# Optimization experiments

Hardware: AMD Instinct MI355X
Metric: run time of the kernel (lower is better)

The kernel has to match this reference:

```python
import jax, jax.numpy as jnp
from jax import lax
import numpy as np

B, L, D = 32, 128, 6          # programs, statements per program, tree depth
T = 2 ** D - 1                # nodes per statement tree (complete binary tree)
V, E, C, H = 50000, 128, 128, 256  # vocab, embed dim, encode dim, gru hidden


def setup_inputs():
    key = jax.random.key(0)
    ks = jax.random.split(key, 12)
    s = 0.05
    return {
        "tokens": jax.random.randint(ks[0], (B, L, T), 0, V),
        "emb": jax.random.normal(ks[1], (V, E), jnp.float32) * s,
        "Wc": jax.random.normal(ks[2], (C, E), jnp.float32) * s,
        "bc": jax.random.normal(ks[3], (C,), jnp.float32) * s,
        "Wih_f": jax.random.normal(ks[4], (3 * H, C), jnp.float32) * s,
        "Whh_f": jax.random.normal(ks[5], (3 * H, H), jnp.float32) * s,
        "bih_f": jax.random.normal(ks[6], (3 * H,), jnp.float32) * s,
        "bhh_f": jax.random.normal(ks[7], (3 * H,), jnp.float32) * s,
        "Wih_b": jax.random.normal(ks[8], (3 * H, C), jnp.float32) * s,
        "Whh_b": jax.random.normal(ks[9], (3 * H, H), jnp.float32) * s,
        "bih_b": jax.random.normal(ks[10], (3 * H,), jnp.float32) * s,
        "bhh_b": jax.random.normal(ks[11], (3 * H,), jnp.float32) * s,
    }


def _tree_encode(tokens, emb, Wc, bc):
    # h(node) = W_c(embed(tok)) + sum of children subtree encodings (W_l/W_r unused in source)
    h = jnp.einsum("blte,ce->bltc", emb[tokens], Wc) + bc  # [B,L,T,C]
    for d in range(D - 1, 0, -1):  # deepest level first
        start, n = 2 ** d - 1, 2 ** d
        ch = h[:, :, start:start + n, :]
        ch = ch.reshape(ch.shape[0], ch.shape[1], n // 2, 2, ch.shape[-1]).sum(3)
        p0 = 2 ** (d - 1) - 1
        h = h.at[:, :, p0:p0 + n // 2, :].add(ch)
    # max over all subtree encodings, with zeros included (batch_node starts at 0)
    return jnp.maximum(h.max(axis=2), 0.0)  # [B,L,C]


def _gru_dir(x, Wih, Whh, bih, bhh, reverse):
    # torch GRU gate order: r, z, n
    def step(hp, xt):
        gi = xt @ Wih.T + bih
        gh = hp @ Whh.T + bhh
        ir, iz, inn = jnp.split(gi, 3, -1)
        hr, hz, hn = jnp.split(gh, 3, -1)
        r = jax.nn.sigmoid(ir + hr)
        z = jax.nn.sigmoid(iz + hz)
        nn_ = jnp.tanh(inn + r * hn)
        hnew = (1.0 - z) * nn_ + z * hp
        return hnew, hnew
    xs = jnp.swapaxes(x, 0, 1)  # [L,B,C]
    h0 = jnp.zeros((x.shape[0], Whh.shape[1]), x.dtype)
    _, ys = lax.scan(step, h0, xs, reverse=reverse)
    return jnp.swapaxes(ys, 0, 1)  # [B,L,H]


def reference(tokens, emb, Wc, bc, Wih_f, Whh_f, bih_f, bhh_f, Wih_b, Whh_b, bih_b, bhh_b):
    enc = _tree_encode(tokens, emb, Wc, bc)                       # [B,L,C]
    fwd = _gru_dir(enc, Wih_f, Whh_f, bih_f, bhh_f, reverse=False)
    bwd = _gru_dir(enc, Wih_b, Whh_b, bih_b, bhh_b, reverse=True)
    gru_out = jnp.concatenate([fwd, bwd], axis=-1)                # [B,L,2H]
    return gru_out.max(axis=1)                                    # max-pool over time -> [B,2H]
```

## Files before the change

kernel.cpp:

```cpp
#include <hip/hip_runtime.h>
#include <hip/hip_bf16.h>
#include <hip/hip_fp16.h>
#include <math.h>

#define NV 50000
#define NC 128
#define NH 256
#define NB 32
#define NL 128
#define NT 63
#define G3 768

typedef _Float16 half2_t __attribute__((ext_vector_type(2)));

__device__ __forceinline__ float sigmoidf_(float x) { return 1.0f / (1.0f + expf(-x)); }

__device__ __forceinline__ float fdot2_(unsigned int a, unsigned int b, float c) {
#if __has_builtin(__builtin_amdgcn_fdot2)
  return __builtin_amdgcn_fdot2(__builtin_bit_cast(half2_t, a),
                                __builtin_bit_cast(half2_t, b), c, false);
#else
  half2_t ah = __builtin_bit_cast(half2_t, a);
  half2_t bh = __builtin_bit_cast(half2_t, b);
  return fmaf((float)ah[0], (float)bh[0], fmaf((float)ah[1], (float)bh[1], c));
#endif
}

__global__ __launch_bounds__(256) void gemm_bt_k128(
    const float* __restrict__ A, const float* __restrict__ Bm,
    const float* __restrict__ bias, float* __restrict__ Cm,
    int M, int N) {
  __shared__ __align__(16) float As[64 * 129];
  __shared__ __align__(16) float BsT[128 * 132];
  const int m0 = blockIdx.x * 64;
  const int n0 = blockIdx.y * 128;
  const int tid = threadIdx.x;

#pragma unroll
  for (int i = 0; i < 32; ++i) {
    int e = tid + i * 256;
    int r = e >> 7, k = e & 127;
    int m = m0 + r;
    As[r * 129 + k] = (m < M) ? A[(size_t)m * 128 + k] : 0.0f;
  }
#pragma unroll
  for (int i = 0; i < 64; ++i) {
    int e = tid + i * 256;
    int n = e >> 7, k = e & 127;
    BsT[k * 132 + n] = Bm[(size_t)(n0 + n) * 128 + k];
  }
  __syncthreads();

  const int tn = tid & 15;
  const int tm = tid >> 4;
  const int ml = tm * 4, nl = tn * 8;

  float acc[4][8];
#pragma unroll
  for (int i = 0; i < 4; ++i)
#pragma unroll
    for (int j = 0; j < 8; ++j) acc[i][j] = 0.0f;

#pragma unroll 4
  for (int k = 0; k < 128; ++k) {
    float a0 = As[(ml + 0) * 129 + k];
    float a1 = As[(ml + 1) * 129 + k];
    float a2 = As[(ml + 2) * 129 + k];
    float a3 = As[(ml + 3) * 129 + k];
    float4 b0 = *(const float4*)&BsT[k * 132 + nl];
    float4 b1 = *(const float4*)&BsT[k * 132 + nl + 4];
    const float bv[8] = {b0.x, b0.y, b0.z, b0.w, b1.x, b1.y, b1.z, b1.w};
#pragma unroll
    for (int j = 0; j < 8; ++j) {
      acc[0][j] = fmaf(a0, bv[j], acc[0][j]);
      acc[1][j] = fmaf(a1, bv[j], acc[1][j]);
      acc[2][j] = fmaf(a2, bv[j], acc[2][j]);
      acc[3][j] = fmaf(a3, bv[j], acc[3][j]);
    }
  }

  float bv[8];
#pragma unroll
  for (int j = 0; j < 8; ++j) bv[j] = bias ? bias[n0 + nl + j] : 0.0f;

#pragma unroll
  for (int i = 0; i < 4; ++i) {
    int m = m0 + ml + i;
    if (m < M) {
      float* crow = &Cm[(size_t)m * N + n0 + nl];
#pragma unroll
      for (int j = 0; j < 8; ++j) crow[j] = acc[i][j] + bv[j];
    }
  }
}

__global__ __launch_bounds__(256) void gemm_bt_k128_dual(
    const float* __restrict__ A,
    const float* __restrict__ B0, const float* __restrict__ B1,
    const float* __restrict__ bias0, const float* __restrict__ bias1,
    float* __restrict__ C0, float* __restrict__ C1, int M, int N) {
  const float* __restrict__ Bm = blockIdx.z ? B1 : B0;
  const float* __restrict__ bias = blockIdx.z ? bias1 : bias0;
  float* __restrict__ Cm = blockIdx.z ? C1 : C0;

  __shared__ __align__(16) float As[64 * 129];
  __shared__ __align__(16) float BsT[128 * 132];
  const int m0 = blockIdx.x * 64;
  const int n0 = blockIdx.y * 128;
  const int tid = threadIdx.x;

#pragma unroll
  for (int i = 0; i < 32; ++i) {
    int e = tid + i * 256;
    int r = e >> 7, k = e & 127;
    int m = m0 + r;
    As[r * 129 + k] = (m < M) ? A[(size_t)m * 128 + k] : 0.0f;
  }
#pragma unroll
  for (int i = 0; i < 64; ++i) {
    int e = tid + i * 256;
    int n = e >> 7, k = e & 127;
    BsT[k * 132 + n] = Bm[(size_t)(n0 + n) * 128 + k];
  }
  __syncthreads();

  const int tn = tid & 15;
  const int tm = tid >> 4;
  const int ml = tm * 4, nl = tn * 8;

  float acc[4][8];
#pragma unroll
  for (int i = 0; i < 4; ++i)
#pragma unroll
    for (int j = 0; j < 8; ++j) acc[i][j] = 0.0f;

#pragma unroll 4
  for (int k = 0; k < 128; ++k) {
    float a0 = As[(ml + 0) * 129 + k];
    float a1 = As[(ml + 1) * 129 + k];
    float a2 = As[(ml + 2) * 129 + k];
    float a3 = As[(ml + 3) * 129 + k];
    float4 b0 = *(const float4*)&BsT[k * 132 + nl];
    float4 b1 = *(const float4*)&BsT[k * 132 + nl + 4];
    const float bv[8] = {b0.x, b0.y, b0.z, b0.w, b1.x, b1.y, b1.z, b1.w};
#pragma unroll
    for (int j = 0; j < 8; ++j) {
      acc[0][j] = fmaf(a0, bv[j], acc[0][j]);
      acc[1][j] = fmaf(a1, bv[j], acc[1][j]);
      acc[2][j] = fmaf(a2, bv[j], acc[2][j]);
      acc[3][j] = fmaf(a3, bv[j], acc[3][j]);
    }
  }

  float bv[8];
#pragma unroll
  for (int j = 0; j < 8; ++j) bv[j] = bias[n0 + nl + j];

#pragma unroll
  for (int i = 0; i < 4; ++i) {
    int m = m0 + ml + i;
    if (m < M) {
      float* crow = &Cm[(size_t)m * N + n0 + nl];
#pragma unroll
      for (int j = 0; j < 8; ++j) crow[j] = acc[i][j] + bv[j];
    }
  }
}

__global__ __launch_bounds__(128) void tree_encode(
    const int* __restrict__ tokens, const float* __restrict__ P,
    const float* __restrict__ bc, float* __restrict__ enc) {
  __shared__ int toks[NT];
  const int blk = blockIdx.x;
  const int c = threadIdx.x;
  if (c < NT) toks[c] = tokens[(size_t)blk * NT + c];
  __syncthreads();

  float s[NT];
#pragma unroll
  for (int i = 0; i < NT; ++i) s[i] = P[(size_t)toks[i] * NC + c];
#pragma unroll
  for (int i = 30; i >= 0; --i) s[i] += s[2 * i + 1] + s[2 * i + 2];

  const float bcv = bc[c];
  float m = -1e30f;
#pragma unroll
  for (int i = 0; i < NT; ++i) {
    const float cnt = (i == 0) ? 63.0f
                    : (i < 3)  ? 31.0f
                    : (i < 7)  ? 15.0f
                    : (i < 15) ? 7.0f
                    : (i < 31) ? 3.0f
                               : 1.0f;
    m = fmaxf(m, s[i] + cnt * bcv);
  }
  enc[(size_t)blk * NC + c] = fmaxf(m, 0.0f);
}

__global__ __launch_bounds__(256) void conv_w_pack(
    const float* __restrict__ Wf, const float* __restrict__ Wb,
    uint4* __restrict__ out) {
  int i = blockIdx.x * 256 + threadIdx.x;
  if (i >= 2 * 32 * G3) return;
  int dir = i / (32 * G3);
  int rem = i - dir * 32 * G3;
  int kc = rem / G3;
  int row = rem - kc * G3;
  const float* __restrict__ W = dir ? Wb : Wf;
  const float4 a = *(const float4*)&W[(size_t)row * NH + kc * 8];
  const float4 b = *(const float4*)&W[(size_t)row * NH + kc * 8 + 4];
  __half2 p0 = __floats2half2_rn(a.x, a.y);
  __half2 p1 = __floats2half2_rn(a.z, a.w);
  __half2 p2 = __floats2half2_rn(b.x, b.y);
  __half2 p3 = __floats2half2_rn(b.z, b.w);
  uint4 o;
  o.x = *(unsigned int*)&p0; o.y = *(unsigned int*)&p1;
  o.z = *(unsigned int*)&p2; o.w = *(unsigned int*)&p3;
  out[i] = o;
}

__global__ __launch_bounds__(512, 2) void gru_scan_v4(
    const uint4* __restrict__ Wpk, const float* __restrict__ GI,
    const float* __restrict__ bhh_f, const float* __restrict__ bhh_b,
    float* __restrict__ out) {
  const int dir = blockIdx.x >> 5;
  const int b = blockIdx.x & 31;
  const int tid = threadIdx.x;
  const int c = tid >> 1;
  const int kh = tid & 1;

  __shared__ __align__(16) uint4 hbuf[2][32];

  const uint4* __restrict__ Wd = Wpk + (size_t)dir * 32 * G3;
  uint4 wr[16], wz[16], wn[16];
#pragma unroll
  for (int j = 0; j < 16; ++j) {
    const size_t base = (size_t)(kh * 16 + j) * G3 + c;
    wr[j] = Wd[base];
    wz[j] = Wd[base + NH];
    wn[j] = Wd[base + 2 * NH];
  }
  const float* __restrict__ bhh = dir ? bhh_b : bhh_f;
  const float br = bhh[c], bz = bhh[c + NH], bn = bhh[c + 2 * NH];
  if (tid < 32) ((uint4*)hbuf)[tid] = uint4{0u, 0u, 0u, 0u};

  const float* __restrict__ gi_base =
      GI + ((size_t)dir * NB * NL + (size_t)b * NL) * G3;
  float gir, giz, gin;
  {
    const float* g = gi_base + (size_t)(dir ? NL - 1 : 0) * G3;
    gir = g[c]; giz = g[c + NH]; gin = g[c + 2 * NH];
  }
  float hreg = 0.0f, hmax = -1e30f;
  __syncthreads();

  for (int st = 0; st < NL; ++st) {
    float girN, gizN, ginN;
    {
      const int stn = (st + 1 < NL) ? st + 1 : st;
      const int tn = dir ? (NL - 1 - stn) : stn;
      const float* g = gi_base + (size_t)tn * G3;
      girN = g[c]; gizN = g[c + NH]; ginN = g[c + 2 * NH];
    }
    const uint4* __restrict__ h4 = hbuf[st & 1] + kh * 16;
    float ar = 0.f, az = 0.f, an = 0.f;
#pragma unroll
    for (int j = 0; j < 16; ++j) {
      uint4 hv = h4[j];
      ar = fdot2_(wr[j].x, hv.x, ar); ar = fdot2_(wr[j].y, hv.y, ar);
      ar = fdot2_(wr[j].z, hv.z, ar); ar = fdot2_(wr[j].w, hv.w, ar);
      az = fdot2_(wz[j].x, hv.x, az); az = fdot2_(wz[j].y, hv.y, az);
      az = fdot2_(wz[j].z, hv.z, az); az = fdot2_(wz[j].w, hv.w, az);
      an = fdot2_(wn[j].x, hv.x, an); an = fdot2_(wn[j].y, hv.y, an);
      an = fdot2_(wn[j].z, hv.z, an); an = fdot2_(wn[j].w, hv.w, an);
    }
    ar += __shfl_xor(ar, 1);
    az += __shfl_xor(az, 1);
    an += __shfl_xor(an, 1);
    float r = sigmoidf_(gir + ar + br);
    float z = sigmoidf_(giz + az + bz);
    float n = tanhf(gin + r * (an + bn));
    hreg = (1.0f - z) * n + z * hreg;
    hmax = fmaxf(hmax, hreg);
    if (kh == 0) {
      ((unsigned short*)hbuf[(st + 1) & 1])[c] =
          __half_as_ushort(__float2half_rn(hreg));
    }
    __syncthreads();
    gir = girN; giz = gizN; gin = ginN;
  }
  if (kh == 0) out[(size_t)b * (2 * NH) + (size_t)dir * NH + c] = hmax;
}

extern "C" void kernel_launch(void* const* d_in, const int* in_sizes, int n_in,
                              void* d_out, int out_size, void* d_ws, size_t ws_size,
                              hipStream_t stream) {
  const int*   tokens = (const int*)d_in[0];
  const float* emb    = (const float*)d_in[1];
  const float* Wc     = (const float*)d_in[2];
  const float* bc     = (const float*)d_in[3];
  const float* Wih_f  = (const float*)d_in[4];
  const float* Whh_f  = (const float*)d_in[5];
  const float* bih_f  = (const float*)d_in[6];
  const float* bhh_f  = (const float*)d_in[7];
  const float* Wih_b  = (const float*)d_in[8];
  const float* Whh_b  = (const float*)d_in[9];
  const float* bih_b  = (const float*)d_in[10];
  const float* bhh_b  = (const float*)d_in[11];
  float* out = (float*)d_out;

  float* P   = (float*)d_ws;
  float* enc = P + (size_t)NV * NC;
  float* GI  = enc + (size_t)NB * NL * NC;
  uint4* Wpk = (uint4*)(GI + (size_t)2 * NB * NL * G3);

  conv_w_pack<<<dim3((2 * 32 * G3 + 255) / 256), dim3(256), 0, stream>>>(
      Whh_f, Whh_b, Wpk);
  gemm_bt_k128<<<dim3((NV + 63) / 64, NC / 128), dim3(256), 0, stream>>>(
      emb, Wc, nullptr, P, NV, NC);
  tree_encode<<<dim3(NB * NL), dim3(128), 0, stream>>>(tokens, P, bc, enc);
  gemm_bt_k128_dual<<<dim3(NB * NL / 64, G3 / 128, 2), dim3(256), 0, stream>>>(
      enc, Wih_f, Wih_b, bih_f, bih_b,
      GI, GI + (size_t)NB * NL * G3, NB * NL, G3);
  gru_scan_v4<<<dim3(64), dim3(512), 0, stream>>>(
      Wpk, GI, bhh_f, bhh_b, out);
}
```

Baseline: 324.3 us.

## Restructure GRU scan to 4-way K split with DPP reductions and halve GEMM LDS

The GRU recurrence kernel changes from 2 threads per hidden unit to 4 threads per pair of hidden units, each covering a quarter of K for two output columns. Partial sums are reduced with DPP lane swizzles instead of shuffles, and the LDS hidden buffer is padded to avoid bank conflicts. The weight-pack kernel is rewritten to match the new register layout. The GEMM kernels stage B in two 64-wide K halves, halving B's LDS so more blocks can be resident, at the cost of an extra barrier.

```diff
diff --git a/kernel.cpp b/kernel.cpp
--- a/kernel.cpp
+++ b/kernel.cpp
@@ -26,12 +26,23 @@
 #endif
 }
 
+__device__ __forceinline__ float dpp_xor1_add(float v) {
+  int x = __builtin_amdgcn_update_dpp(0, __builtin_bit_cast(int, v),
+                                      0xB1 , 0xF, 0xF, true);
+  return v + __builtin_bit_cast(float, x);
+}
+__device__ __forceinline__ float dpp_xor2_add(float v) {
+  int x = __builtin_amdgcn_update_dpp(0, __builtin_bit_cast(int, v),
+                                      0x4E , 0xF, 0xF, true);
+  return v + __builtin_bit_cast(float, x);
+}
+
 __global__ __launch_bounds__(256) void gemm_bt_k128(
     const float* __restrict__ A, const float* __restrict__ Bm,
     const float* __restrict__ bias, float* __restrict__ Cm,
     int M, int N) {
   __shared__ __align__(16) float As[64 * 129];
-  __shared__ __align__(16) float BsT[128 * 132];
+  __shared__ __align__(16) float BsT[64 * 132];
   const int m0 = blockIdx.x * 64;
   const int n0 = blockIdx.y * 128;
   const int tid = threadIdx.x;
@@ -43,13 +54,6 @@
     int m = m0 + r;
     As[r * 129 + k] = (m < M) ? A[(size_t)m * 128 + k] : 0.0f;
   }
-#pragma unroll
-  for (int i = 0; i < 64; ++i) {
-    int e = tid + i * 256;
-    int n = e >> 7, k = e & 127;
-    BsT[k * 132 + n] = Bm[(size_t)(n0 + n) * 128 + k];
-  }
-  __syncthreads();
 
   const int tn = tid & 15;
   const int tm = tid >> 4;
@@ -61,21 +65,33 @@
 #pragma unroll
     for (int j = 0; j < 8; ++j) acc[i][j] = 0.0f;
 
+#pragma unroll
+  for (int h = 0; h < 2; ++h) {
+    if (h) __syncthreads();
+#pragma unroll
+    for (int i = 0; i < 32; ++i) {
+      int e = tid + i * 256;
+      int n = e >> 6, kk = e & 63;
+      BsT[kk * 132 + n] = Bm[(size_t)(n0 + n) * 128 + h * 64 + kk];
+    }
+    __syncthreads();
 #pragma unroll 4
-  for (int k = 0; k < 128; ++k) {
-    float a0 = As[(ml + 0) * 129 + k];
-    float a1 = As[(ml + 1) * 129 + k];
-    float a2 = As[(ml + 2) * 129 + k];
-    float a3 = As[(ml + 3) * 129 + k];
-    float4 b0 = *(const float4*)&BsT[k * 132 + nl];
-    float4 b1 = *(const float4*)&BsT[k * 132 + nl + 4];
-    const float bv[8] = {b0.x, b0.y, b0.z, b0.w, b1.x, b1.y, b1.z, b1.w};
-#pragma unroll
-    for (int j = 0; j < 8; ++j) {
-      acc[0][j] = fmaf(a0, bv[j], acc[0][j]);
-      acc[1][j] = fmaf(a1, bv[j], acc[1][j]);
-      acc[2][j] = fmaf(a2, bv[j], acc[2][j]);
-      acc[3][j] = fmaf(a3, bv[j], acc[3][j]);
+    for (int kk = 0; kk < 64; ++kk) {
+      const int k = h * 64 + kk;
+      float a0 = As[(ml + 0) * 129 + k];
+      float a1 = As[(ml + 1) * 129 + k];
+      float a2 = As[(ml + 2) * 129 + k];
+      float a3 = As[(ml + 3) * 129 + k];
+      float4 b0 = *(const float4*)&BsT[kk * 132 + nl];
+      float4 b1 = *(const float4*)&BsT[kk * 132 + nl + 4];
+      const float bv[8] = {b0.x, b0.y, b0.z, b0.w, b1.x, b1.y, b1.z, b1.w};
+#pragma unroll
+      for (int j = 0; j < 8; ++j) {
+        acc[0][j] = fmaf(a0, bv[j], acc[0][j]);
+        acc[1][j] = fmaf(a1, bv[j], acc[1][j]);
+        acc[2][j] = fmaf(a2, bv[j], acc[2][j]);
+        acc[3][j] = fmaf(a3, bv[j], acc[3][j]);
+      }
     }
   }
 
@@ -104,7 +120,7 @@
   float* __restrict__ Cm = blockIdx.z ? C1 : C0;
 
   __shared__ __align__(16) float As[64 * 129];
-  __shared__ __align__(16) float BsT[128 * 132];
+  __shared__ __align__(16) float BsT[64 * 132];
   const int m0 = blockIdx.x * 64;
   const int n0 = blockIdx.y * 128;
   const int tid = threadIdx.x;
@@ -116,13 +132,6 @@
     int m = m0 + r;
     As[r * 129 + k] = (m < M) ? A[(size_t)m * 128 + k] : 0.0f;
   }
-#pragma unroll
-  for (int i = 0; i < 64; ++i) {
-    int e = tid + i * 256;
-    int n = e >> 7, k = e & 127;
-    BsT[k * 132 + n] = Bm[(size_t)(n0 + n) * 128 + k];
-  }
-  __syncthreads();
 
   const int tn = tid & 15;
   const int tm = tid >> 4;
@@ -134,21 +143,33 @@
 #pragma unroll
     for (int j = 0; j < 8; ++j) acc[i][j] = 0.0f;
 
+#pragma unroll
+  for (int h = 0; h < 2; ++h) {
+    if (h) __syncthreads();
+#pragma unroll
+    for (int i = 0; i < 32; ++i) {
+      int e = tid + i * 256;
+      int n = e >> 6, kk = e & 63;
+      BsT[kk * 132 + n] = Bm[(size_t)(n0 + n) * 128 + h * 64 + kk];
+    }
+    __syncthreads();
 #pragma unroll 4
-  for (int k = 0; k < 128; ++k) {
-    float a0 = As[(ml + 0) * 129 + k];
-    float a1 = As[(ml + 1) * 129 + k];
-    float a2 = As[(ml + 2) * 129 + k];
-    float a3 = As[(ml + 3) * 129 + k];
-    float4 b0 = *(const float4*)&BsT[k * 132 + nl];
-    float4 b1 = *(const float4*)&BsT[k * 132 + nl + 4];
-    const float bv[8] = {b0.x, b0.y, b0.z, b0.w, b1.x, b1.y, b1.z, b1.w};
-#pragma unroll
-    for (int j = 0; j < 8; ++j) {
-      acc[0][j] = fmaf(a0, bv[j], acc[0][j]);
-      acc[1][j] = fmaf(a1, bv[j], acc[1][j]);
-      acc[2][j] = fmaf(a2, bv[j], acc[2][j]);
-      acc[3][j] = fmaf(a3, bv[j], acc[3][j]);
+    for (int kk = 0; kk < 64; ++kk) {
+      const int k = h * 64 + kk;
+      float a0 = As[(ml + 0) * 129 + k];
+      float a1 = As[(ml + 1) * 129 + k];
+      float a2 = As[(ml + 2) * 129 + k];
+      float a3 = As[(ml + 3) * 129 + k];
+      float4 b0 = *(const float4*)&BsT[kk * 132 + nl];
+      float4 b1 = *(const float4*)&BsT[kk * 132 + nl + 4];
+      const float bv[8] = {b0.x, b0.y, b0.z, b0.w, b1.x, b1.y, b1.z, b1.w};
+#pragma unroll
+      for (int j = 0; j < 8; ++j) {
+        acc[0][j] = fmaf(a0, bv[j], acc[0][j]);
+        acc[1][j] = fmaf(a1, bv[j], acc[1][j]);
+        acc[2][j] = fmaf(a2, bv[j], acc[2][j]);
+        acc[3][j] = fmaf(a3, bv[j], acc[3][j]);
+      }
     }
   }
 
@@ -201,11 +222,17 @@
     const float* __restrict__ Wf, const float* __restrict__ Wb,
     uint4* __restrict__ out) {
   int i = blockIdx.x * 256 + threadIdx.x;
-  if (i >= 2 * 32 * G3) return;
-  int dir = i / (32 * G3);
-  int rem = i - dir * 32 * G3;
-  int kc = rem / G3;
-  int row = rem - kc * G3;
+  if (i >= 2 * 48 * 512) return;
+  const int dir = i / (48 * 512);
+  int rem = i - dir * (48 * 512);
+  const int jj = rem >> 9;
+  const int gq = rem & 511;
+  const int g = gq >> 2;
+  const int q = gq & 3;
+  const int rowSel = jj >> 3;
+  const int j = jj & 7;
+  const int row = (rowSel % 3) * 256 + (rowSel / 3) * 128 + g;
+  const int kc = q * 8 + j;
   const float* __restrict__ W = dir ? Wb : Wf;
   const float4 a = *(const float4*)&W[(size_t)row * NH + kc * 8];
   const float4 b = *(const float4*)&W[(size_t)row * NH + kc * 8 + 4];
@@ -219,77 +246,91 @@
   out[i] = o;
 }
 
-__global__ __launch_bounds__(512, 2) void gru_scan_v4(
+__global__ __launch_bounds__(512, 2) void gru_scan_v5(
     const uint4* __restrict__ Wpk, const float* __restrict__ GI,
     const float* __restrict__ bhh_f, const float* __restrict__ bhh_b,
     float* __restrict__ out) {
   const int dir = blockIdx.x >> 5;
   const int b = blockIdx.x & 31;
   const int tid = threadIdx.x;
-  const int c = tid >> 1;
-  const int kh = tid & 1;
-
-  __shared__ __align__(16) uint4 hbuf[2][32];
-
-  const uint4* __restrict__ Wd = Wpk + (size_t)dir * 32 * G3;
-  uint4 wr[16], wz[16], wn[16];
-#pragma unroll
-  for (int j = 0; j < 16; ++j) {
-    const size_t base = (size_t)(kh * 16 + j) * G3 + c;
-    wr[j] = Wd[base];
-    wz[j] = Wd[base + NH];
-    wn[j] = Wd[base + 2 * NH];
-  }
+  const int g = tid >> 2;
+  const int q = tid & 3;
+
+  __shared__ __align__(16) unsigned short hbuf[2][288];
+
+  const uint4* __restrict__ Wd = Wpk + (size_t)dir * 48 * 512;
+  uint4 w[48];
+#pragma unroll
+  for (int jj = 0; jj < 48; ++jj) w[jj] = Wd[(size_t)jj * 512 + tid];
+
+  const bool owner = ((q & 1) == 0);
+  const int c = g + (q >> 1) * 128;
   const float* __restrict__ bhh = dir ? bhh_b : bhh_f;
-  const float br = bhh[c], bz = bhh[c + NH], bn = bhh[c + 2 * NH];
-  if (tid < 32) ((uint4*)hbuf)[tid] = uint4{0u, 0u, 0u, 0u};
+  float br = 0.f, bz = 0.f, bn = 0.f;
+  if (owner) {
+    br = bhh[c]; bz = bhh[c + NH]; bn = bhh[c + 2 * NH];
+  }
+  if (tid < 144) ((unsigned int*)&hbuf[0][0])[tid] = 0u;
 
   const float* __restrict__ gi_base =
       GI + ((size_t)dir * NB * NL + (size_t)b * NL) * G3;
-  float gir, giz, gin;
-  {
-    const float* g = gi_base + (size_t)(dir ? NL - 1 : 0) * G3;
-    gir = g[c]; giz = g[c + NH]; gin = g[c + 2 * NH];
+  float gir = 0.f, giz = 0.f, gin = 0.f;
+  if (owner) {
+    const float* gi = gi_base + (size_t)(dir ? NL - 1 : 0) * G3;
+    gir = gi[c]; giz = gi[c + NH]; gin = gi[c + 2 * NH];
   }
   float hreg = 0.0f, hmax = -1e30f;
   __syncthreads();
 
   for (int st = 0; st < NL; ++st) {
-    float girN, gizN, ginN;
-    {
+    float girN = 0.f, gizN = 0.f, ginN = 0.f;
+    if (owner) {
       const int stn = (st + 1 < NL) ? st + 1 : st;
-      const int tn = dir ? (NL - 1 - stn) : stn;
-      const float* g = gi_base + (size_t)tn * G3;
-      girN = g[c]; gizN = g[c + NH]; ginN = g[c + 2 * NH];
-    }
-    const uint4* __restrict__ h4 = hbuf[st & 1] + kh * 16;
-    float ar = 0.f, az = 0.f, an = 0.f;
-#pragma unroll
-    for (int j = 0; j < 16; ++j) {
-      uint4 hv = h4[j];
-      ar = fdot2_(wr[j].x, hv.x, ar); ar = fdot2_(wr[j].y, hv.y, ar);
-      ar = fdot2_(wr[j].z, hv.z, ar); ar = fdot2_(wr[j].w, hv.w, ar);
-      az = fdot2_(wz[j].x, hv.x, az); az = fdot2_(wz[j].y, hv.y, az);
-      az = fdot2_(wz[j].z, hv.z, az); az = fdot2_(wz[j].w, hv.w, az);
-      an = fdot2_(wn[j].x, hv.x, an); an = fdot2_(wn[j].y, hv.y, an);
-      an = fdot2_(wn[j].z, hv.z, an); an = fdot2_(wn[j].w, hv.w, an);
-    }
-    ar += __shfl_xor(ar, 1);
-    az += __shfl_xor(az, 1);
-    an += __shfl_xor(an, 1);
-    float r = sigmoidf_(gir + ar + br);
-    float z = sigmoidf_(giz + az + bz);
-    float n = tanhf(gin + r * (an + bn));
-    hreg = (1.0f - z) * n + z * hreg;
-    hmax = fmaxf(hmax, hreg);
-    if (kh == 0) {
-      ((unsigned short*)hbuf[(st + 1) & 1])[c] =
+      const int t = dir ? (NL - 1 - stn) : stn;
+      const float* gi = gi_base + (size_t)t * G3;
+      girN = gi[c]; gizN = gi[c + NH]; ginN = gi[c + 2 * NH];
+    }
+    const uint4* __restrict__ hp =
+        (const uint4*)((const char*)&hbuf[st & 1][0] + q * 144);
+    float a0 = 0.f, a1 = 0.f, a2 = 0.f, a3 = 0.f, a4 = 0.f, a5 = 0.f;
+#pragma unroll
+    for (int j = 0; j < 8; ++j) {
+      uint4 hv = hp[j];
+      a0 = fdot2_(w[j].x, hv.x, a0);      a0 = fdot2_(w[j].y, hv.y, a0);
+      a0 = fdot2_(w[j].z, hv.z, a0);      a0 = fdot2_(w[j].w, hv.w, a0);
+      a1 = fdot2_(w[8+j].x, hv.x, a1);    a1 = fdot2_(w[8+j].y, hv.y, a1);
+      a1 = fdot2_(w[8+j].z, hv.z, a1);    a1 = fdot2_(w[8+j].w, hv.w, a1);
+      a2 = fdot2_(w[16+j].x, hv.x, a2);   a2 = fdot2_(w[16+j].y, hv.y, a2);
+      a2 = fdot2_(w[16+j].z, hv.z, a2);   a2 = fdot2_(w[16+j].w, hv.w, a2);
+      a3 = fdot2_(w[24+j].x, hv.x, a3);   a3 = fdot2_(w[24+j].y, hv.y, a3);
+      a3 = fdot2_(w[24+j].z, hv.z, a3);   a3 = fdot2_(w[24+j].w, hv.w, a3);
+      a4 = fdot2_(w[32+j].x, hv.x, a4);   a4 = fdot2_(w[32+j].y, hv.y, a4);
+      a4 = fdot2_(w[32+j].z, hv.z, a4);   a4 = fdot2_(w[32+j].w, hv.w, a4);
+      a5 = fdot2_(w[40+j].x, hv.x, a5);   a5 = fdot2_(w[40+j].y, hv.y, a5);
+      a5 = fdot2_(w[40+j].z, hv.z, a5);   a5 = fdot2_(w[40+j].w, hv.w, a5);
+    }
+    a0 = dpp_xor2_add(dpp_xor1_add(a0));
+    a1 = dpp_xor2_add(dpp_xor1_add(a1));
+    a2 = dpp_xor2_add(dpp_xor1_add(a2));
+    a3 = dpp_xor2_add(dpp_xor1_add(a3));
+    a4 = dpp_xor2_add(dpp_xor1_add(a4));
+    a5 = dpp_xor2_add(dpp_xor1_add(a5));
+    if (owner) {
+      const float sr = (q >> 1) ? a3 : a0;
+      const float sz = (q >> 1) ? a4 : a1;
+      const float sn = (q >> 1) ? a5 : a2;
+      float r = sigmoidf_(gir + sr + br);
+      float z = sigmoidf_(giz + sz + bz);
+      float n = tanhf(gin + r * (sn + bn));
+      hreg = (1.0f - z) * n + z * hreg;
+      hmax = fmaxf(hmax, hreg);
+      hbuf[(st + 1) & 1][(c >> 6) * 72 + (c & 63)] =
           __half_as_ushort(__float2half_rn(hreg));
     }
     __syncthreads();
     gir = girN; giz = gizN; gin = ginN;
   }
-  if (kh == 0) out[(size_t)b * (2 * NH) + (size_t)dir * NH + c] = hmax;
+  if (owner) out[(size_t)b * (2 * NH) + (size_t)dir * NH + c] = hmax;
 }
 
 extern "C" void kernel_launch(void* const* d_in, const int* in_sizes, int n_in,
@@ -314,7 +355,7 @@
   float* GI  = enc + (size_t)NB * NL * NC;
   uint4* Wpk = (uint4*)(GI + (size_t)2 * NB * NL * G3);
 
-  conv_w_pack<<<dim3((2 * 32 * G3 + 255) / 256), dim3(256), 0, stream>>>(
+  conv_w_pack<<<dim3((2 * 48 * 512 + 255) / 256), dim3(256), 0, stream>>>(
       Whh_f, Whh_b, Wpk);
   gemm_bt_k128<<<dim3((NV + 63) / 64, NC / 128), dim3(256), 0, stream>>>(
       emb, Wc, nullptr, P, NV, NC);
@@ -322,6 +363,6 @@
   gemm_bt_k128_dual<<<dim3(NB * NL / 64, G3 / 128, 2), dim3(256), 0, stream>>>(
       enc, Wih_f, Wih_b, bih_f, bih_b,
       GI, GI + (size_t)NB * NL * G3, NB * NL, G3);
-  gru_scan_v4<<<dim3(64), dim3(512), 0, stream>>>(
+  gru_scan_v5<<<dim3(64), dim3(512), 0, stream>>>(
       Wpk, GI, bhh_f, bhh_b, out);
 }
```

Result: no change. 323.2 us (-0.4%).

## Give each GRU thread a full hidden row and split GEMM B tile in halves

Applied to the files above, without the earlier changes.

The GRU scan now uses 256 threads per block, with each thread holding all 96 packed fp16 weight vectors for its hidden unit, where before two threads each held half a row. This removes the cross-lane shuffle reduction and halves the threads per block. Two interleaved accumulators per gate shorten the fdot2 dependency chains. The weight pack layout is changed to match. Separately, both input GEMMs now stage the B tile in two K halves to halve its LDS footprint, which may raise occupancy but adds a barrier. The risk is very high VGPR pressure (384 registers of weights per thread) and fewer waves to hide latency on the serial recurrence.

```diff
diff --git a/kernel.cpp b/kernel.cpp
--- a/kernel.cpp
+++ b/kernel.cpp
@@ -31,7 +31,7 @@
     const float* __restrict__ bias, float* __restrict__ Cm,
     int M, int N) {
   __shared__ __align__(16) float As[64 * 129];
-  __shared__ __align__(16) float BsT[128 * 132];
+  __shared__ __align__(16) float BsT[64 * 132];
   const int m0 = blockIdx.x * 64;
   const int n0 = blockIdx.y * 128;
   const int tid = threadIdx.x;
@@ -43,13 +43,6 @@
     int m = m0 + r;
     As[r * 129 + k] = (m < M) ? A[(size_t)m * 128 + k] : 0.0f;
   }
-#pragma unroll
-  for (int i = 0; i < 64; ++i) {
-    int e = tid + i * 256;
-    int n = e >> 7, k = e & 127;
-    BsT[k * 132 + n] = Bm[(size_t)(n0 + n) * 128 + k];
-  }
-  __syncthreads();
 
   const int tn = tid & 15;
   const int tm = tid >> 4;
@@ -61,21 +54,33 @@
 #pragma unroll
     for (int j = 0; j < 8; ++j) acc[i][j] = 0.0f;
 
+#pragma unroll
+  for (int h = 0; h < 2; ++h) {
+    if (h) __syncthreads();
+#pragma unroll
+    for (int i = 0; i < 32; ++i) {
+      int e = tid + i * 256;
+      int n = e >> 6, kk = e & 63;
+      BsT[kk * 132 + n] = Bm[(size_t)(n0 + n) * 128 + h * 64 + kk];
+    }
+    __syncthreads();
 #pragma unroll 4
-  for (int k = 0; k < 128; ++k) {
-    float a0 = As[(ml + 0) * 129 + k];
-    float a1 = As[(ml + 1) * 129 + k];
-    float a2 = As[(ml + 2) * 129 + k];
-    float a3 = As[(ml + 3) * 129 + k];
-    float4 b0 = *(const float4*)&BsT[k * 132 + nl];
-    float4 b1 = *(const float4*)&BsT[k * 132 + nl + 4];
-    const float bv[8] = {b0.x, b0.y, b0.z, b0.w, b1.x, b1.y, b1.z, b1.w};
-#pragma unroll
-    for (int j = 0; j < 8; ++j) {
-      acc[0][j] = fmaf(a0, bv[j], acc[0][j]);
-      acc[1][j] = fmaf(a1, bv[j], acc[1][j]);
-      acc[2][j] = fmaf(a2, bv[j], acc[2][j]);
-      acc[3][j] = fmaf(a3, bv[j], acc[3][j]);
+    for (int kk = 0; kk < 64; ++kk) {
+      const int k = h * 64 + kk;
+      float a0 = As[(ml + 0) * 129 + k];
+      float a1 = As[(ml + 1) * 129 + k];
+      float a2 = As[(ml + 2) * 129 + k];
+      float a3 = As[(ml + 3) * 129 + k];
+      float4 b0 = *(const float4*)&BsT[kk * 132 + nl];
+      float4 b1 = *(const float4*)&BsT[kk * 132 + nl + 4];
+      const float bv[8] = {b0.x, b0.y, b0.z, b0.w, b1.x, b1.y, b1.z, b1.w};
+#pragma unroll
+      for (int j = 0; j < 8; ++j) {
+        acc[0][j] = fmaf(a0, bv[j], acc[0][j]);
+        acc[1][j] = fmaf(a1, bv[j], acc[1][j]);
+        acc[2][j] = fmaf(a2, bv[j], acc[2][j]);
+        acc[3][j] = fmaf(a3, bv[j], acc[3][j]);
+      }
     }
   }
 
@@ -104,7 +109,7 @@
   float* __restrict__ Cm = blockIdx.z ? C1 : C0;
 
   __shared__ __align__(16) float As[64 * 129];
-  __shared__ __align__(16) float BsT[128 * 132];
+  __shared__ __align__(16) float BsT[64 * 132];
   const int m0 = blockIdx.x * 64;
   const int n0 = blockIdx.y * 128;
   const int tid = threadIdx.x;
@@ -116,13 +121,6 @@
     int m = m0 + r;
     As[r * 129 + k] = (m < M) ? A[(size_t)m * 128 + k] : 0.0f;
   }
-#pragma unroll
-  for (int i = 0; i < 64; ++i) {
-    int e = tid + i * 256;
-    int n = e >> 7, k = e & 127;
-    BsT[k * 132 + n] = Bm[(size_t)(n0 + n) * 128 + k];
-  }
-  __syncthreads();
 
   const int tn = tid & 15;
   const int tm = tid >> 4;
@@ -134,21 +132,33 @@
 #pragma unroll
     for (int j = 0; j < 8; ++j) acc[i][j] = 0.0f;
 
+#pragma unroll
+  for (int h = 0; h < 2; ++h) {
+    if (h) __syncthreads();
+#pragma unroll
+    for (int i = 0; i < 32; ++i) {
+      int e = tid + i * 256;
+      int n = e >> 6, kk = e & 63;
+      BsT[kk * 132 + n] = Bm[(size_t)(n0 + n) * 128 + h * 64 + kk];
+    }
+    __syncthreads();
 #pragma unroll 4
-  for (int k = 0; k < 128; ++k) {
-    float a0 = As[(ml + 0) * 129 + k];
-    float a1 = As[(ml + 1) * 129 + k];
-    float a2 = As[(ml + 2) * 129 + k];
-    float a3 = As[(ml + 3) * 129 + k];
-    float4 b0 = *(const float4*)&BsT[k * 132 + nl];
-    float4 b1 = *(const float4*)&BsT[k * 132 + nl + 4];
-    const float bv[8] = {b0.x, b0.y, b0.z, b0.w, b1.x, b1.y, b1.z, b1.w};
-#pragma unroll
-    for (int j = 0; j < 8; ++j) {
-      acc[0][j] = fmaf(a0, bv[j], acc[0][j]);
-      acc[1][j] = fmaf(a1, bv[j], acc[1][j]);
-      acc[2][j] = fmaf(a2, bv[j], acc[2][j]);
-      acc[3][j] = fmaf(a3, bv[j], acc[3][j]);
+    for (int kk = 0; kk < 64; ++kk) {
+      const int k = h * 64 + kk;
+      float a0 = As[(ml + 0) * 129 + k];
+      float a1 = As[(ml + 1) * 129 + k];
+      float a2 = As[(ml + 2) * 129 + k];
+      float a3 = As[(ml + 3) * 129 + k];
+      float4 b0 = *(const float4*)&BsT[kk * 132 + nl];
+      float4 b1 = *(const float4*)&BsT[kk * 132 + nl + 4];
+      const float bv[8] = {b0.x, b0.y, b0.z, b0.w, b1.x, b1.y, b1.z, b1.w};
+#pragma unroll
+      for (int j = 0; j < 8; ++j) {
+        acc[0][j] = fmaf(a0, bv[j], acc[0][j]);
+        acc[1][j] = fmaf(a1, bv[j], acc[1][j]);
+        acc[2][j] = fmaf(a2, bv[j], acc[2][j]);
+        acc[3][j] = fmaf(a3, bv[j], acc[3][j]);
+      }
     }
   }
 
@@ -201,14 +211,17 @@
     const float* __restrict__ Wf, const float* __restrict__ Wb,
     uint4* __restrict__ out) {
   int i = blockIdx.x * 256 + threadIdx.x;
-  if (i >= 2 * 32 * G3) return;
-  int dir = i / (32 * G3);
-  int rem = i - dir * 32 * G3;
-  int kc = rem / G3;
-  int row = rem - kc * G3;
+  if (i >= 2 * 3 * 32 * 256) return;
+  const int dir = i / 24576;
+  int rem = i - dir * 24576;
+  const int rs = rem >> 13;
+  rem &= 8191;
+  const int j = rem >> 8;
+  const int c = rem & 255;
+  const int row = rs * 256 + c;
   const float* __restrict__ W = dir ? Wb : Wf;
-  const float4 a = *(const float4*)&W[(size_t)row * NH + kc * 8];
-  const float4 b = *(const float4*)&W[(size_t)row * NH + kc * 8 + 4];
+  const float4 a = *(const float4*)&W[(size_t)row * NH + j * 8];
+  const float4 b = *(const float4*)&W[(size_t)row * NH + j * 8 + 4];
   __half2 p0 = __floats2half2_rn(a.x, a.y);
   __half2 p1 = __floats2half2_rn(a.z, a.w);
   __half2 p2 = __floats2half2_rn(b.x, b.y);
@@ -219,30 +232,24 @@
   out[i] = o;
 }
 
-__global__ __launch_bounds__(512, 2) void gru_scan_v4(
+__global__ __launch_bounds__(256, 1) void gru_scan_v6(
     const uint4* __restrict__ Wpk, const float* __restrict__ GI,
     const float* __restrict__ bhh_f, const float* __restrict__ bhh_b,
     float* __restrict__ out) {
   const int dir = blockIdx.x >> 5;
   const int b = blockIdx.x & 31;
-  const int tid = threadIdx.x;
-  const int c = tid >> 1;
-  const int kh = tid & 1;
+  const int c = threadIdx.x;
 
   __shared__ __align__(16) uint4 hbuf[2][32];
 
-  const uint4* __restrict__ Wd = Wpk + (size_t)dir * 32 * G3;
-  uint4 wr[16], wz[16], wn[16];
-#pragma unroll
-  for (int j = 0; j < 16; ++j) {
-    const size_t base = (size_t)(kh * 16 + j) * G3 + c;
-    wr[j] = Wd[base];
-    wz[j] = Wd[base + NH];
-    wn[j] = Wd[base + 2 * NH];
-  }
+  const uint4* __restrict__ Wd = Wpk + (size_t)dir * 96 * 256;
+  uint4 w[96];
+#pragma unroll
+  for (int j = 0; j < 96; ++j) w[j] = Wd[(size_t)j * 256 + c];
+
   const float* __restrict__ bhh = dir ? bhh_b : bhh_f;
   const float br = bhh[c], bz = bhh[c + NH], bn = bhh[c + 2 * NH];
-  if (tid < 32) ((uint4*)hbuf)[tid] = uint4{0u, 0u, 0u, 0u};
+  if (threadIdx.x < 32) ((uint4*)hbuf)[threadIdx.x] = uint4{0u, 0u, 0u, 0u};
 
   const float* __restrict__ gi_base =
       GI + ((size_t)dir * NB * NL + (size_t)b * NL) * G3;
@@ -258,38 +265,33 @@
     float girN, gizN, ginN;
     {
       const int stn = (st + 1 < NL) ? st + 1 : st;
-      const int tn = dir ? (NL - 1 - stn) : stn;
-      const float* g = gi_base + (size_t)tn * G3;
+      const int t = dir ? (NL - 1 - stn) : stn;
+      const float* g = gi_base + (size_t)t * G3;
       girN = g[c]; gizN = g[c + NH]; ginN = g[c + 2 * NH];
     }
-    const uint4* __restrict__ h4 = hbuf[st & 1] + kh * 16;
-    float ar = 0.f, az = 0.f, an = 0.f;
-#pragma unroll
-    for (int j = 0; j < 16; ++j) {
+    const uint4* __restrict__ h4 = hbuf[st & 1];
+    float ar0 = 0.f, ar1 = 0.f, az0 = 0.f, az1 = 0.f, an0 = 0.f, an1 = 0.f;
+#pragma unroll
+    for (int j = 0; j < 32; ++j) {
       uint4 hv = h4[j];
-      ar = fdot2_(wr[j].x, hv.x, ar); ar = fdot2_(wr[j].y, hv.y, ar);
-      ar = fdot2_(wr[j].z, hv.z, ar); ar = fdot2_(wr[j].w, hv.w, ar);
-      az = fdot2_(wz[j].x, hv.x, az); az = fdot2_(wz[j].y, hv.y, az);
-      az = fdot2_(wz[j].z, hv.z, az); az = fdot2_(wz[j].w, hv.w, az);
-      an = fdot2_(wn[j].x, hv.x, an); an = fdot2_(wn[j].y, hv.y, an);
-      an = fdot2_(wn[j].z, hv.z, an); an = fdot2_(wn[j].w, hv.w, an);
-    }
-    ar += __shfl_xor(ar, 1);
-    az += __shfl_xor(az, 1);
-    an += __shfl_xor(an, 1);
-    float r = sigmoidf_(gir + ar + br);
-    float z = sigmoidf_(giz + az + bz);
-    float n = tanhf(gin + r * (an + bn));
+      ar0 = fdot2_(w[j].x, hv.x, ar0);       ar1 = fdot2_(w[j].y, hv.y, ar1);
+      ar0 = fdot2_(w[j].z, hv.z, ar0);       ar1 = fdot2_(w[j].w, hv.w, ar1);
+      az0 = fdot2_(w[32 + j].x, hv.x, az0);  az1 = fdot2_(w[32 + j].y, hv.y, az1);
+      az0 = fdot2_(w[32 + j].z, hv.z, az0);  az1 = fdot2_(w[32 + j].w, hv.w, az1);
+      an0 = fdot2_(w[64 + j].x, hv.x, an0);  an1 = fdot2_(w[64 + j].y, hv.y, an1);
+      an0 = fdot2_(w[64 + j].z, hv.z, an0);  an1 = fdot2_(w[64 + j].w, hv.w, an1);
+    }
+    float r = sigmoidf_(gir + (ar0 + ar1) + br);
+    float z = sigmoidf_(giz + (az0 + az1) + bz);
+    float n = tanhf(gin + r * ((an0 + an1) + bn));
     hreg = (1.0f - z) * n + z * hreg;
     hmax = fmaxf(hmax, hreg);
-    if (kh == 0) {
-      ((unsigned short*)hbuf[(st + 1) & 1])[c] =
-          __half_as_ushort(__float2half_rn(hreg));
-    }
+    ((unsigned short*)&hbuf[(st + 1) & 1][0])[c] =
+        __half_as_ushort(__float2half_rn(hreg));
     __syncthreads();
     gir = girN; giz = gizN; gin = ginN;
   }
-  if (kh == 0) out[(size_t)b * (2 * NH) + (size_t)dir * NH + c] = hmax;
+  out[(size_t)b * (2 * NH) + (size_t)dir * NH + c] = hmax;
 }
 
 extern "C" void kernel_launch(void* const* d_in, const int* in_sizes, int n_in,
@@ -314,7 +316,7 @@
   float* GI  = enc + (size_t)NB * NL * NC;
   uint4* Wpk = (uint4*)(GI + (size_t)2 * NB * NL * G3);
 
-  conv_w_pack<<<dim3((2 * 32 * G3 + 255) / 256), dim3(256), 0, stream>>>(
+  conv_w_pack<<<dim3((2 * 3 * 32 * 256 + 255) / 256), dim3(256), 0, stream>>>(
       Whh_f, Whh_b, Wpk);
   gemm_bt_k128<<<dim3((NV + 63) / 64, NC / 128), dim3(256), 0, stream>>>(
       emb, Wc, nullptr, P, NV, NC);
@@ -322,6 +324,6 @@
   gemm_bt_k128_dual<<<dim3(NB * NL / 64, G3 / 128, 2), dim3(256), 0, stream>>>(
       enc, Wih_f, Wih_b, bih_f, bih_b,
       GI, GI + (size_t)NB * NL * G3, NB * NL, G3);
-  gru_scan_v4<<<dim3(64), dim3(512), 0, stream>>>(
+  gru_scan_v6<<<dim3(64), dim3(256), 0, stream>>>(
       Wpk, GI, bhh_f, bhh_b, out);
 }
```

Result: slower. 381.3 us (+17.5%).
